# Optimization experiments

Hardware: AMD Instinct MI355X
Metric: run time of the kernel (lower is better)

The kernel has to match this reference:

```python
import jax, jax.numpy as jnp
import numpy as np

N_NODES = 100000
N_EDGES = 1600000
D_IN = 128
D_OUT = 128


def setup_inputs() -> dict:
    key = jax.random.key(0)
    k1, k2, k3, k4 = jax.random.split(key, 4)
    feat = jax.random.normal(k1, (N_NODES, D_IN), dtype=jnp.float32)
    # xavier_uniform on [D_IN, D_OUT]
    limit = float(np.sqrt(6.0 / (D_IN + D_OUT)))
    weight = jax.random.uniform(k2, (D_IN, D_OUT), minval=-limit, maxval=limit, dtype=jnp.float32)
    bias = jnp.zeros((D_OUT,), dtype=jnp.float32)
    src = jax.random.randint(k3, (N_EDGES,), 0, N_NODES, dtype=jnp.int32)
    dst = jax.random.randint(k4, (N_EDGES,), 0, N_NODES, dtype=jnp.int32)
    return {"feat": feat, "weight": weight, "bias": bias, "src": src, "dst": dst}


def reference(feat, weight, bias, src, dst):
    n = feat.shape[0]
    # in-degree of each node (number of incoming edges)
    deg = jax.ops.segment_sum(jnp.ones_like(dst, dtype=feat.dtype), dst, num_segments=n)
    norm = jnp.power(jnp.clip(deg, 1.0), -0.5)[:, None]  # [N, 1]
    # pre-normalize source features
    h = feat * norm
    # copy_src + sum aggregation: scatter-add messages from src to dst
    agg = jax.ops.segment_sum(h[src], dst, num_segments=n)  # [N, D_IN]
    # in_feats == out_feats -> matmul after aggregation (the else-branch)
    rst = jnp.matmul(agg, weight)
    rst = rst * norm + bias
    return rst
```

## Files before the change

kernel.cpp:

```cpp
#include <hip/hip_runtime.h>

#define D 128
#define BSHIFT 7
#define BNODES 128
#define BMASK 127
#define NB_MAX 1024
#define STRIDE 2944
#define BIN_CHUNK 4096

typedef unsigned int uint;
typedef __attribute__((ext_vector_type(8))) short bf16x8;
typedef __attribute__((ext_vector_type(4))) float f32x4;

__device__ inline uint bf16_rne(float x) {
    uint u = __float_as_uint(x);
    return (u + 0x7fffu + ((u >> 16) & 1u)) >> 16;
}
__device__ inline uint pack2(float lo, float hi) {
    return bf16_rne(lo) | (bf16_rne(hi) << 16);
}

__global__ void __launch_bounds__(256) bin_kernel(const int* __restrict__ src,
                                                  const int* __restrict__ dst,
                                                  int* __restrict__ bucket_cur,
                                                  uint* __restrict__ binned,
                                                  const float* __restrict__ W,
                                                  uint4* __restrict__ wpack,
                                                  int n_edges, int nchunks) {
    int t = threadIdx.x;
    if (blockIdx.x == (uint)nchunks) {
        for (int idx = t; idx < 2048; idx += 256) {
            int lane = idx & 63;
            int ks = (idx >> 6) & 3;
            int ct = idx >> 8;
            int col = ct * 16 + (lane & 15);
            int k0 = ks * 32 + (lane >> 4) * 8;
            uint4 u;
            u.x = pack2(W[(k0 + 0) * D + col], W[(k0 + 1) * D + col]);
            u.y = pack2(W[(k0 + 2) * D + col], W[(k0 + 3) * D + col]);
            u.z = pack2(W[(k0 + 4) * D + col], W[(k0 + 5) * D + col]);
            u.w = pack2(W[(k0 + 6) * D + col], W[(k0 + 7) * D + col]);
            wpack[idx] = u;
        }
        return;
    }

    __shared__ int h[NB_MAX];
    __shared__ int base[NB_MAX];
    long long e0 = (long long)blockIdx.x * BIN_CHUNK;
    for (int j = t; j < NB_MAX; j += 256) h[j] = 0;
    __syncthreads();

    int d[16], s[16];
#pragma unroll
    for (int k = 0; k < 16; ++k) {
        long long idx = e0 + k * 256 + t;
        if (idx < n_edges) {
            d[k] = dst[idx];
            s[k] = src[idx];
            atomicAdd(&h[d[k] >> BSHIFT], 1);
        } else {
            d[k] = -1;
        }
    }
    __syncthreads();
    for (int j = t; j < NB_MAX; j += 256) {
        int c = h[j];
        base[j] = c ? atomicAdd(&bucket_cur[j], c) : 0;
        h[j] = 0;
    }
    __syncthreads();
#pragma unroll
    for (int k = 0; k < 16; ++k) {
        if (d[k] >= 0) {
            int b = d[k] >> BSHIFT;
            int r = base[b] + atomicAdd(&h[b], 1);
            if (r < STRIDE)
                binned[(size_t)b * STRIDE + r] =
                    ((uint)s[k] << BSHIFT) | (uint)(d[k] & BMASK);
        }
    }
}

__global__ void __launch_bounds__(256) fill2_kernel(
        const int* __restrict__ bucket_cur, uint* __restrict__ csr,
        const float* __restrict__ feat, float* __restrict__ norm,
        int* __restrict__ row_start, int* __restrict__ degp,
        uint* __restrict__ h32, int n_nodes) {
    __shared__ uint sbin[STRIDE];
    __shared__ int deg[BNODES];
    __shared__ int rs[BNODES];
    __shared__ int cur[BNODES];
    __shared__ float snorm[BNODES];
    int b = blockIdx.x;
    int t = threadIdx.x;
    int cnt = bucket_cur[b];
    if (cnt > STRIDE) cnt = STRIDE;
    size_t gbase = (size_t)b * STRIDE;

    for (int k = t; k < cnt; k += 256) sbin[k] = csr[gbase + k];
    if (t < BNODES) deg[t] = 0;
    __syncthreads();
    for (int k = t; k < cnt; k += 256) atomicAdd(&deg[sbin[k] & BMASK], 1);
    __syncthreads();

    int v = 0;
    if (t < BNODES) {
        v = deg[t];
        rs[t] = v;
    }
    __syncthreads();
    for (int o = 1; o < BNODES; o <<= 1) {
        int a = (t < BNODES && t >= o) ? rs[t - o] : 0;
        __syncthreads();
        if (t < BNODES) rs[t] += a;
        __syncthreads();
    }
    if (t < BNODES) {
        int excl = rs[t] - v;
        rs[t] = excl;
        cur[t] = 0;
        int node = b * BNODES + t;
        float nm = 0.f;
        if (node < n_nodes) {
            row_start[node] = (int)gbase + excl;
            degp[node] = v;
            nm = rsqrtf(fmaxf((float)v, 1.0f));
            norm[node] = nm;
        }
        snorm[t] = nm;
    }
    __syncthreads();

    for (int k = t; k < cnt; k += 256) {
        uint p = sbin[k];
        int dl = p & BMASK;
        int r = atomicAdd(&cur[dl], 1);
        csr[gbase + rs[dl] + r] = p >> BSHIFT;
    }

    int base_node = b * BNODES;
    int rows = n_nodes - base_node;
    if (rows > BNODES) rows = BNODES;
    for (int u = t; u < rows * 32; u += 256) {
        int row = u >> 5;
        int part = u & 31;
        int node = base_node + row;
        float nm = snorm[row];
        float4 f = *(const float4*)(feat + (size_t)node * D + part * 4);
        uint2 o;
        o.x = pack2(f.x * nm, f.y * nm);
        o.y = pack2(f.z * nm, f.w * nm);
        *(uint2*)(h32 + (size_t)node * 64 + part * 2) = o;
    }
}

#define UNPACK_ADD(u)                              \
    acc[0] += __uint_as_float((u).x << 16);        \
    acc[1] += __uint_as_float((u).x & 0xffff0000u);\
    acc[2] += __uint_as_float((u).y << 16);        \
    acc[3] += __uint_as_float((u).y & 0xffff0000u);\
    acc[4] += __uint_as_float((u).z << 16);        \
    acc[5] += __uint_as_float((u).z & 0xffff0000u);\
    acc[6] += __uint_as_float((u).w << 16);        \
    acc[7] += __uint_as_float((u).w & 0xffff0000u);

#define LDP 132

__global__ void __launch_bounds__(256) gather_mm_kernel(
        const uint4* __restrict__ h128, const uint* __restrict__ csr,
        const int* __restrict__ row_start, const int* __restrict__ degp,
        const float* __restrict__ norm, const uint4* __restrict__ wpack,
        const float* __restrict__ bias, float* __restrict__ out, int n) {
    __shared__ float As[16][LDP];
    int t = threadIdx.x;
    int lane = t & 63;
    int w = t >> 6;
    int r0 = blockIdx.x * 16;
    int g = lane >> 4;
    int c = lane & 15;

    for (int q = 0; q < 4; ++q) {
        int local = w * 4 + q;
        int i = r0 + local;
        float acc[8];
#pragma unroll
        for (int j = 0; j < 8; ++j) acc[j] = 0.f;

        if (i < n) {
            int beg = row_start[i];
            int end = beg + degp[i];
            for (int base = beg; base < end; base += 64) {
                int nk = end - base;
                if (nk > 64) nk = 64;
                int epre = (base + lane < end) ? (int)csr[base + lane] : 0;
                int k = 0;
                int kfull = nk & ~7;
                for (; k < kfull; k += 8) {
                    int s0 = __shfl(epre, k + g, 64);
                    int s1 = __shfl(epre, k + 4 + g, 64);
                    uint4 u0 = h128[(size_t)s0 * 16 + c];
                    uint4 u1 = h128[(size_t)s1 * 16 + c];
                    UNPACK_ADD(u0);
                    UNPACK_ADD(u1);
                }
                if (k < nk) {
                    int e0 = k + g;
                    int e1 = k + 4 + g;
                    int s0 = __shfl(epre, e0 & 63, 64);
                    int s1 = __shfl(epre, e1 & 63, 64);
                    uint4 z = {0u, 0u, 0u, 0u};
                    uint4 u0 = (e0 < nk) ? h128[(size_t)s0 * 16 + c] : z;
                    uint4 u1 = (e1 < nk) ? h128[(size_t)s1 * 16 + c] : z;
                    UNPACK_ADD(u0);
                    UNPACK_ADD(u1);
                }
            }
        }
#pragma unroll
        for (int j = 0; j < 8; ++j) {
            acc[j] += __shfl_xor(acc[j], 16, 64);
            acc[j] += __shfl_xor(acc[j], 32, 64);
        }
        if (g == 0) {
            float4 lo = {acc[0], acc[1], acc[2], acc[3]};
            float4 hi = {acc[4], acc[5], acc[6], acc[7]};
            *(float4*)&As[local][8 * c] = lo;
            *(float4*)&As[local][8 * c + 4] = hi;
        }
    }
    __syncthreads();

    uint4 afr[4];
#pragma unroll
    for (int ks = 0; ks < 4; ++ks) {
        const float* ap = &As[c][ks * 32 + g * 8];
        float4 f0 = *(const float4*)ap;
        float4 f1 = *(const float4*)(ap + 4);
        afr[ks].x = pack2(f0.x, f0.y);
        afr[ks].y = pack2(f0.z, f0.w);
        afr[ks].z = pack2(f1.x, f1.y);
        afr[ks].w = pack2(f1.z, f1.w);
    }

    float nm[4];
    int grow[4];
#pragma unroll
    for (int r = 0; r < 4; ++r) {
        grow[r] = r0 + g * 4 + r;
        int rc = grow[r] < n ? grow[r] : n - 1;
        nm[r] = norm[rc];
    }

#pragma unroll
    for (int cc = 0; cc < 2; ++cc) {
        int ct = 2 * w + cc;
        f32x4 acc = {0.f, 0.f, 0.f, 0.f};
#pragma unroll
        for (int ks = 0; ks < 4; ++ks) {
            uint4 bu = wpack[(ct * 4 + ks) * 64 + lane];
            acc = __builtin_amdgcn_mfma_f32_16x16x32_bf16(
                *(bf16x8*)&afr[ks], *(bf16x8*)&bu, acc, 0, 0, 0);
        }
        float bv = bias[ct * 16 + c];
#pragma unroll
        for (int r = 0; r < 4; ++r)
            if (grow[r] < n)
                out[(size_t)grow[r] * D + ct * 16 + c] = acc[r] * nm[r] + bv;
    }
}

extern "C" void kernel_launch(void* const* d_in, const int* in_sizes, int n_in,
                              void* d_out, int out_size, void* d_ws, size_t ws_size,
                              hipStream_t stream) {
    const float* feat   = (const float*)d_in[0];
    const float* weight = (const float*)d_in[1];
    const float* bias   = (const float*)d_in[2];
    const int*   src    = (const int*)d_in[3];
    const int*   dst    = (const int*)d_in[4];
    float* out = (float*)d_out;

    int n_nodes = in_sizes[0] / D;
    int n_edges = in_sizes[3];
    int nb = (n_nodes + BNODES - 1) >> BSHIFT;
    int nchunks = (n_edges + BIN_CHUNK - 1) / BIN_CHUNK;

    float* norm       = (float*)d_ws;
    int*   degp       = (int*)(norm + n_nodes);
    int*   row_start  = degp + n_nodes;
    int*   bucket_cur = row_start + n_nodes;
    uint*  csr        = (uint*)(bucket_cur + NB_MAX);
    uint*  h32        = csr + (size_t)nb * STRIDE;
    uint4* wpack      = (uint4*)(h32 + (size_t)n_nodes * 64);

    hipMemsetAsync(bucket_cur, 0, NB_MAX * sizeof(int), stream);

    bin_kernel<<<nchunks + 1, 256, 0, stream>>>(src, dst, bucket_cur, csr,
                                                weight, wpack, n_edges, nchunks);
    fill2_kernel<<<nb, 256, 0, stream>>>(bucket_cur, csr, feat, norm, row_start,
                                         degp, h32, n_nodes);
    gather_mm_kernel<<<(n_nodes + 15) / 16, 256, 0, stream>>>(
        (const uint4*)h32, csr, row_start, degp, norm, wpack, bias, out, n_nodes);
}
```

Before: 132.6 us.

## Apply weight matmul before aggregation and gather transformed features

```diff
diff --git a/kernel.cpp b/kernel.cpp
--- a/kernel.cpp
+++ b/kernel.cpp
@@ -84,14 +84,11 @@
 
 __global__ void __launch_bounds__(256) fill2_kernel(
         const int* __restrict__ bucket_cur, uint* __restrict__ csr,
-        const float* __restrict__ feat, float* __restrict__ norm,
-        int* __restrict__ row_start, int* __restrict__ degp,
-        uint* __restrict__ h32, int n_nodes) {
+        int* __restrict__ row_start, int* __restrict__ degp, int n_nodes) {
     __shared__ uint sbin[STRIDE];
     __shared__ int deg[BNODES];
     __shared__ int rs[BNODES];
     __shared__ int cur[BNODES];
-    __shared__ float snorm[BNODES];
     int b = blockIdx.x;
     int t = threadIdx.x;
     int cnt = bucket_cur[b];
@@ -121,14 +118,10 @@
         rs[t] = excl;
         cur[t] = 0;
         int node = b * BNODES + t;
-        float nm = 0.f;
         if (node < n_nodes) {
             row_start[node] = (int)gbase + excl;
             degp[node] = v;
-            nm = rsqrtf(fmaxf((float)v, 1.0f));
-            norm[node] = nm;
-        }
-        snorm[t] = nm;
+        }
     }
     __syncthreads();
 
@@ -138,20 +131,75 @@
         int r = atomicAdd(&cur[dl], 1);
         csr[gbase + rs[dl] + r] = p >> BSHIFT;
     }
-
-    int base_node = b * BNODES;
-    int rows = n_nodes - base_node;
-    if (rows > BNODES) rows = BNODES;
-    for (int u = t; u < rows * 32; u += 256) {
-        int row = u >> 5;
-        int part = u & 31;
-        int node = base_node + row;
-        float nm = snorm[row];
-        float4 f = *(const float4*)(feat + (size_t)node * D + part * 4);
-        uint2 o;
-        o.x = pack2(f.x * nm, f.y * nm);
-        o.y = pack2(f.z * nm, f.w * nm);
-        *(uint2*)(h32 + (size_t)node * 64 + part * 2) = o;
+}
+
+#define GP_ROWS 64
+#define GLDP 132
+__global__ void __launch_bounds__(256) gemm_prep_kernel(
+        const float* __restrict__ feat, const int* __restrict__ degp,
+        const uint4* __restrict__ wpack, uint* __restrict__ g32, int n) {
+    __shared__ float As[GP_ROWS][GLDP];
+    int t = threadIdx.x;
+    int lane = t & 63;
+    int w = t >> 6;
+    int r0 = blockIdx.x * GP_ROWS;
+
+    for (int idx = t; idx < GP_ROWS * 32; idx += 256) {
+        int row = idx >> 5;
+        int p = idx & 31;
+        int gr = r0 + row;
+        if (gr >= n) gr = n - 1;
+        float4 f = *(const float4*)(feat + (size_t)gr * D + p * 4);
+        *(float4*)&As[row][p * 4] = f;
+    }
+    __syncthreads();
+
+    int c = lane & 15;
+    int g = lane >> 4;
+    int rbase = w * 16;
+
+    uint4 afr[4];
+#pragma unroll
+    for (int ks = 0; ks < 4; ++ks) {
+        const float* ap = &As[rbase + c][ks * 32 + g * 8];
+        float4 f0 = *(const float4*)ap;
+        float4 f1 = *(const float4*)(ap + 4);
+        afr[ks].x = pack2(f0.x, f0.y);
+        afr[ks].y = pack2(f0.z, f0.w);
+        afr[ks].z = pack2(f1.x, f1.y);
+        afr[ks].w = pack2(f1.z, f1.w);
+    }
+
+    float nm[4];
+#pragma unroll
+    for (int r = 0; r < 4; ++r) {
+        int gr = r0 + rbase + g * 4 + r;
+        int rc = gr < n ? gr : n - 1;
+        nm[r] = rsqrtf(fmaxf((float)degp[rc], 1.0f));
+    }
+
+#pragma unroll
+    for (int ct = 0; ct < 8; ++ct) {
+        f32x4 acc = {0.f, 0.f, 0.f, 0.f};
+#pragma unroll
+        for (int ks = 0; ks < 4; ++ks) {
+            uint4 bu = wpack[(ct * 4 + ks) * 64 + lane];
+            acc = __builtin_amdgcn_mfma_f32_16x16x32_bf16(
+                *(bf16x8*)&afr[ks], *(bf16x8*)&bu, acc, 0, 0, 0);
+        }
+#pragma unroll
+        for (int r = 0; r < 4; ++r)
+            As[rbase + g * 4 + r][ct * 16 + c] = acc[r] * nm[r];
+    }
+
+    for (int idx = lane; idx < 16 * 64; idx += 64) {
+        int row = idx >> 6;
+        int j = idx & 63;
+        int gr = r0 + rbase + row;
+        if (gr < n) {
+            uint vpk = pack2(As[rbase + row][2 * j], As[rbase + row][2 * j + 1]);
+            g32[(size_t)gr * 64 + j] = vpk;
+        }
     }
 }
 
@@ -165,108 +213,72 @@
     acc[6] += __uint_as_float((u).w << 16);        \
     acc[7] += __uint_as_float((u).w & 0xffff0000u);
 
-#define LDP 132
-
-__global__ void __launch_bounds__(256) gather_mm_kernel(
-        const uint4* __restrict__ h128, const uint* __restrict__ csr,
+__global__ void __launch_bounds__(256) gather_out_kernel(
+        const uint4* __restrict__ g128, const uint* __restrict__ csr,
         const int* __restrict__ row_start, const int* __restrict__ degp,
-        const float* __restrict__ norm, const uint4* __restrict__ wpack,
         const float* __restrict__ bias, float* __restrict__ out, int n) {
-    __shared__ float As[16][LDP];
-    int t = threadIdx.x;
-    int lane = t & 63;
-    int w = t >> 6;
-    int r0 = blockIdx.x * 16;
+    int lane = threadIdx.x & 63;
+    int wid = threadIdx.x >> 6;
+    int i = blockIdx.x * 4 + wid;
+    if (i >= n) return;
     int g = lane >> 4;
     int c = lane & 15;
-
-    for (int q = 0; q < 4; ++q) {
-        int local = w * 4 + q;
-        int i = r0 + local;
-        float acc[8];
-#pragma unroll
-        for (int j = 0; j < 8; ++j) acc[j] = 0.f;
-
-        if (i < n) {
-            int beg = row_start[i];
-            int end = beg + degp[i];
-            for (int base = beg; base < end; base += 64) {
-                int nk = end - base;
-                if (nk > 64) nk = 64;
-                int epre = (base + lane < end) ? (int)csr[base + lane] : 0;
-                int k = 0;
-                int kfull = nk & ~7;
-                for (; k < kfull; k += 8) {
-                    int s0 = __shfl(epre, k + g, 64);
-                    int s1 = __shfl(epre, k + 4 + g, 64);
-                    uint4 u0 = h128[(size_t)s0 * 16 + c];
-                    uint4 u1 = h128[(size_t)s1 * 16 + c];
-                    UNPACK_ADD(u0);
-                    UNPACK_ADD(u1);
-                }
-                if (k < nk) {
-                    int e0 = k + g;
-                    int e1 = k + 4 + g;
-                    int s0 = __shfl(epre, e0 & 63, 64);
-                    int s1 = __shfl(epre, e1 & 63, 64);
-                    uint4 z = {0u, 0u, 0u, 0u};
-                    uint4 u0 = (e0 < nk) ? h128[(size_t)s0 * 16 + c] : z;
-                    uint4 u1 = (e1 < nk) ? h128[(size_t)s1 * 16 + c] : z;
-                    UNPACK_ADD(u0);
-                    UNPACK_ADD(u1);
-                }
-            }
-        }
-#pragma unroll
-        for (int j = 0; j < 8; ++j) {
-            acc[j] += __shfl_xor(acc[j], 16, 64);
-            acc[j] += __shfl_xor(acc[j], 32, 64);
-        }
-        if (g == 0) {
-            float4 lo = {acc[0], acc[1], acc[2], acc[3]};
-            float4 hi = {acc[4], acc[5], acc[6], acc[7]};
-            *(float4*)&As[local][8 * c] = lo;
-            *(float4*)&As[local][8 * c + 4] = hi;
-        }
-    }
-    __syncthreads();
-
-    uint4 afr[4];
-#pragma unroll
-    for (int ks = 0; ks < 4; ++ks) {
-        const float* ap = &As[c][ks * 32 + g * 8];
-        float4 f0 = *(const float4*)ap;
-        float4 f1 = *(const float4*)(ap + 4);
-        afr[ks].x = pack2(f0.x, f0.y);
-        afr[ks].y = pack2(f0.z, f0.w);
-        afr[ks].z = pack2(f1.x, f1.y);
-        afr[ks].w = pack2(f1.z, f1.w);
-    }
-
-    float nm[4];
-    int grow[4];
-#pragma unroll
-    for (int r = 0; r < 4; ++r) {
-        grow[r] = r0 + g * 4 + r;
-        int rc = grow[r] < n ? grow[r] : n - 1;
-        nm[r] = norm[rc];
-    }
-
-#pragma unroll
-    for (int cc = 0; cc < 2; ++cc) {
-        int ct = 2 * w + cc;
-        f32x4 acc = {0.f, 0.f, 0.f, 0.f};
-#pragma unroll
-        for (int ks = 0; ks < 4; ++ks) {
-            uint4 bu = wpack[(ct * 4 + ks) * 64 + lane];
-            acc = __builtin_amdgcn_mfma_f32_16x16x32_bf16(
-                *(bf16x8*)&afr[ks], *(bf16x8*)&bu, acc, 0, 0, 0);
-        }
-        float bv = bias[ct * 16 + c];
-#pragma unroll
-        for (int r = 0; r < 4; ++r)
-            if (grow[r] < n)
-                out[(size_t)grow[r] * D + ct * 16 + c] = acc[r] * nm[r] + bv;
+    float4 b_lo = *(const float4*)(bias + 8 * c);
+    float4 b_hi = *(const float4*)(bias + 8 * c + 4);
+
+    int beg = row_start[i];
+    int dv = degp[i];
+    int end = beg + dv;
+    float acc[8];
+#pragma unroll
+    for (int j = 0; j < 8; ++j) acc[j] = 0.f;
+
+    for (int base = beg; base < end; base += 64) {
+        int nk = end - base;
+        if (nk > 64) nk = 64;
+        int epre = (base + lane < end) ? (int)csr[base + lane] : 0;
+        int k = 0;
+        int kfull = nk & ~7;
+        for (; k < kfull; k += 8) {
+            int s0 = __shfl(epre, k + g, 64);
+            int s1 = __shfl(epre, k + 4 + g, 64);
+            uint4 u0 = g128[(size_t)s0 * 16 + c];
+            uint4 u1 = g128[(size_t)s1 * 16 + c];
+            UNPACK_ADD(u0);
+            UNPACK_ADD(u1);
+        }
+        if (k < nk) {
+            int e0 = k + g;
+            int e1 = k + 4 + g;
+            int s0 = __shfl(epre, e0 & 63, 64);
+            int s1 = __shfl(epre, e1 & 63, 64);
+            uint4 z = {0u, 0u, 0u, 0u};
+            uint4 u0 = (e0 < nk) ? g128[(size_t)s0 * 16 + c] : z;
+            uint4 u1 = (e1 < nk) ? g128[(size_t)s1 * 16 + c] : z;
+            UNPACK_ADD(u0);
+            UNPACK_ADD(u1);
+        }
+    }
+
+#pragma unroll
+    for (int j = 0; j < 8; ++j) {
+        acc[j] += __shfl_xor(acc[j], 16, 64);
+        acc[j] += __shfl_xor(acc[j], 32, 64);
+    }
+    if (g == 0) {
+        float nrm = rsqrtf(fmaxf((float)dv, 1.0f));
+        float4 lo, hi;
+        lo.x = acc[0] * nrm + b_lo.x;
+        lo.y = acc[1] * nrm + b_lo.y;
+        lo.z = acc[2] * nrm + b_lo.z;
+        lo.w = acc[3] * nrm + b_lo.w;
+        hi.x = acc[4] * nrm + b_hi.x;
+        hi.y = acc[5] * nrm + b_hi.y;
+        hi.z = acc[6] * nrm + b_hi.z;
+        hi.w = acc[7] * nrm + b_hi.w;
+        float* orow = out + (size_t)i * D + 8 * c;
+        *(float4*)orow = lo;
+        *(float4*)(orow + 4) = hi;
     }
 }
 
@@ -285,20 +297,21 @@
     int nb = (n_nodes + BNODES - 1) >> BSHIFT;
     int nchunks = (n_edges + BIN_CHUNK - 1) / BIN_CHUNK;
 
-    float* norm       = (float*)d_ws;
-    int*   degp       = (int*)(norm + n_nodes);
+    int*   degp       = (int*)d_ws;
     int*   row_start  = degp + n_nodes;
     int*   bucket_cur = row_start + n_nodes;
     uint*  csr        = (uint*)(bucket_cur + NB_MAX);
-    uint*  h32        = csr + (size_t)nb * STRIDE;
-    uint4* wpack      = (uint4*)(h32 + (size_t)n_nodes * 64);
+    uint*  g32        = csr + (size_t)nb * STRIDE;
+    uint4* wpack      = (uint4*)(g32 + (size_t)n_nodes * 64);
 
     hipMemsetAsync(bucket_cur, 0, NB_MAX * sizeof(int), stream);
 
     bin_kernel<<<nchunks + 1, 256, 0, stream>>>(src, dst, bucket_cur, csr,
                                                 weight, wpack, n_edges, nchunks);
-    fill2_kernel<<<nb, 256, 0, stream>>>(bucket_cur, csr, feat, norm, row_start,
-                                         degp, h32, n_nodes);
-    gather_mm_kernel<<<(n_nodes + 15) / 16, 256, 0, stream>>>(
-        (const uint4*)h32, csr, row_start, degp, norm, wpack, bias, out, n_nodes);
-}
+    fill2_kernel<<<nb, 256, 0, stream>>>(bucket_cur, csr, row_start, degp,
+                                         n_nodes);
+    gemm_prep_kernel<<<(n_nodes + GP_ROWS - 1) / GP_ROWS, 256, 0, stream>>>(
+        feat, degp, wpack, g32, n_nodes);
+    gather_out_kernel<<<(n_nodes + 3) / 4, 256, 0, stream>>>(
+        (const uint4*)g32, csr, row_start, degp, bias, out, n_nodes);
+}
```

Measured after the change: 139.0 us. 4.8% more time.
